# Performance work log

Measured on AMD Instinct MI355X. Metric: run time of the kernel, lower is better.

Reference implementation:

```python
import jax, jax.numpy as jnp
import numpy as np

N_EMBD = 384
HEAD_SIZE = 64
B, T = 16, 2048


def setup_inputs() -> dict:
    key = jax.random.key(0)
    ks = jax.random.split(key, 7)
    s = 1.0 / np.sqrt(N_EMBD)
    return {
        "x": jax.random.normal(ks[0], (B, T, N_EMBD), dtype=jnp.float32),
        "Wq": jax.random.uniform(ks[1], (N_EMBD, HEAD_SIZE), jnp.float32, -s, s),
        "bq": jax.random.uniform(ks[2], (HEAD_SIZE,), jnp.float32, -s, s),
        "Wk": jax.random.uniform(ks[3], (N_EMBD, HEAD_SIZE), jnp.float32, -s, s),
        "bk": jax.random.uniform(ks[4], (HEAD_SIZE,), jnp.float32, -s, s),
        "Wv": jax.random.uniform(ks[5], (N_EMBD, HEAD_SIZE), jnp.float32, -s, s),
        "bv": jax.random.uniform(ks[6], (HEAD_SIZE,), jnp.float32, -s, s),
    }


def reference(x, Wq, bq, Wk, bk, Wv, bv):
    # QKV projections: [B,T,C] @ [C,H] -> [B,T,H]
    q = x @ Wq + bq
    k = x @ Wk + bk
    v = x @ Wv + bv
    scale = k.shape[-1] ** (-0.5)
    # NOTE: original forward applies NO causal mask (tril buffer unused).
    scores = jnp.einsum("bqh,bkh->bqk", q, k) * scale  # [B,T,T]
    wmap = jax.nn.softmax(scores, axis=-1)
    # dropout is identity in eval mode
    out = jnp.einsum("bqk,bkh->bqh", wmap, v)  # [B,T,H]
    return out
```

## Files before the change

### kernel.cpp

```cpp
#include <hip/hip_runtime.h>
#include <hip/hip_bf16.h>
#include <cstdint>

typedef unsigned short u16;
typedef __attribute__((ext_vector_type(8))) short short8;
typedef __attribute__((ext_vector_type(4))) short short4v;
typedef __attribute__((ext_vector_type(4))) float f32x4;

#define MFMA16(a, b, c) __builtin_amdgcn_mfma_f32_16x16x32_bf16((a), (b), (c), 0, 0, 0)

constexpr int Bn   = 16;
constexpr int Tn   = 2048;
constexpr int Cn   = 384;
constexpr int Hn   = 64;
constexpr long NTOK = (long)Bn * Tn;
constexpr long NELT = NTOK * Hn;
constexpr int SPLITS = 4;
constexpr int NT_PER = 32 / SPLITS;

#define QSCALE 0.18033688011112042f

__device__ __forceinline__ u16 f2bf(float f) {
  union { float f; uint32_t u; } c; c.f = f;
  uint32_t u = c.u;
  return (u16)((u + 0x7fffu + ((u >> 16) & 1u)) >> 16);
}

__device__ __forceinline__ uint32_t pkbf(float a, float b) {
  uint32_t d;
  asm("v_cvt_pk_bf16_f32 %0, %1, %2" : "=v"(d) : "v"(a), "v"(b));
  return d;
}

__device__ __forceinline__ short8 ldx8(const float* p) {
  const float4 f0 = *reinterpret_cast<const float4*>(p);
  const float4 f1 = *reinterpret_cast<const float4*>(p + 4);
  union { short8 s8; uint32_t u[4]; } r;
  r.u[0] = pkbf(f0.x, f0.y); r.u[1] = pkbf(f0.z, f0.w);
  r.u[2] = pkbf(f1.x, f1.y); r.u[3] = pkbf(f1.z, f1.w);
  return r.s8;
}

__device__ __forceinline__ void gl16(const u16* g, const u16* l) {
  __builtin_amdgcn_global_load_lds(
      (const __attribute__((address_space(1))) void*)g,
      (__attribute__((address_space(3))) void*)l, 16, 0, 0);
}

__global__ __launch_bounds__(256) void wtrans(
    const float* __restrict__ Wq, const float* __restrict__ Wk,
    const float* __restrict__ Wv, u16* __restrict__ wtd)
{
  __shared__ u16 tile[64][65];
  const int m  = blockIdx.x / 6;
  const int kc = blockIdx.x % 6;
  const float* W = (m == 0) ? Wq : (m == 1) ? Wk : Wv;
  const int t = threadIdx.x;

  {
    const int kr = t >> 2, seg = t & 3;
    const float* src = W + (size_t)(kc * 64 + kr) * Hn + seg * 16;
    #pragma unroll
    for (int j = 0; j < 4; ++j) {
      const float4 f = *reinterpret_cast<const float4*>(src + j * 4);
      u16* p = &tile[kr][seg * 16 + j * 4];
      p[0] = f2bf(f.x); p[1] = f2bf(f.y); p[2] = f2bf(f.z); p[3] = f2bf(f.w);
    }
  }
  __syncthreads();
  {
    const int hr = t >> 2, seg = t & 3;
    union { short8 s; u16 u[8]; } o0, o1;
    #pragma unroll
    for (int j = 0; j < 8; ++j) o0.u[j] = tile[seg * 16 + j][hr];
    #pragma unroll
    for (int j = 0; j < 8; ++j) o1.u[j] = tile[seg * 16 + 8 + j][hr];
    u16* dst = wtd + ((size_t)m * 64 + hr) * Cn + kc * 64 + seg * 16;
    *reinterpret_cast<short8*>(dst)     = o0.s;
    *reinterpret_cast<short8*>(dst + 8) = o1.s;
  }
}

__global__ __launch_bounds__(256, 2) void qkv_proj(
    const float* __restrict__ x, const u16* __restrict__ wtd,
    const float* __restrict__ bq, const float* __restrict__ bk,
    const float* __restrict__ bv,
    u16* __restrict__ oq, u16* __restrict__ ok, u16* __restrict__ ovt)
{
  __shared__ u16 wbuf[3][3 * 64 * 64];

  const int t    = threadIdx.x;
  const int lane = t & 63;
  const int w    = t >> 6;
  const int l15  = lane & 15;
  const int lh   = lane >> 4;
  const long r0  = (long)blockIdx.x * 64;

  int srcoff[6];
  #pragma unroll
  for (int i = 0; i < 6; ++i) {
    const int g = i * 256 + t;
    const int r = g >> 3, c = g & 7;
    srcoff[i] = r * Cn + ((c ^ (r & 7)) << 3);
  }
  const int ldsb = w * 64 * 8;

  const float* xrow = x + (r0 + w * 16 + l15) * Cn;

  short8 aCur0 = ldx8(xrow + lh * 8);
  short8 aCur1 = ldx8(xrow + 32 + lh * 8);
  short8 aNxt0, aNxt1;

  const int cks0 = ((lh)     ^ (l15 & 7)) << 3;
  const int cks1 = ((lh + 4) ^ (l15 & 7)) << 3;

  f32x4 acc[3][4];
  #pragma unroll
  for (int m = 0; m < 3; ++m)
    #pragma unroll
    for (int n = 0; n < 4; ++n) acc[m][n] = f32x4{0.f, 0.f, 0.f, 0.f};

  #pragma unroll
  for (int i = 0; i < 6; ++i)
    gl16(wtd + srcoff[i], &wbuf[0][(i * 256) * 8 + ldsb]);
  #pragma unroll
  for (int i = 0; i < 6; ++i)
    gl16(wtd + 64 + srcoff[i], &wbuf[1][(i * 256) * 8 + ldsb]);
  asm volatile("s_waitcnt vmcnt(6)" ::: "memory");
  __builtin_amdgcn_s_barrier();
  __builtin_amdgcn_sched_barrier(0);

  for (int kc = 0; kc < 6; ++kc) {
    const int cb = kc % 3;
    const int sb = (kc + 2) % 3;
    if (kc + 2 < 6) {
      #pragma unroll
      for (int i = 0; i < 6; ++i)
        gl16(wtd + (kc + 2) * 64 + srcoff[i], &wbuf[sb][(i * 256) * 8 + ldsb]);
    }
    if (kc + 1 < 6) {
      const float* p = xrow + (kc + 1) * 64 + lh * 8;
      aNxt0 = ldx8(p);
      aNxt1 = ldx8(p + 32);
    }

    const u16* wc = &wbuf[cb][0];
    #pragma unroll
    for (int m = 0; m < 3; ++m)
      #pragma unroll
      for (int n = 0; n < 4; ++n) {
        const int row = m * 64 + n * 16 + l15;
        const short8 b0 = *reinterpret_cast<const short8*>(&wc[row * 64 + cks0]);
        acc[m][n] = MFMA16(aCur0, b0, acc[m][n]);
        const short8 b1 = *reinterpret_cast<const short8*>(&wc[row * 64 + cks1]);
        acc[m][n] = MFMA16(aCur1, b1, acc[m][n]);
      }

    if (kc + 1 < 6) {
      if (kc + 2 < 6) asm volatile("s_waitcnt vmcnt(10)" ::: "memory");
      else            asm volatile("s_waitcnt vmcnt(4)"  ::: "memory");
      __builtin_amdgcn_s_barrier();
      __builtin_amdgcn_sched_barrier(0);
      aCur0 = aNxt0;
      aCur1 = aNxt1;
    }
  }

  {
    const float* bias[2] = {bq, bk};
    u16*         dst[2]  = {oq, ok};
    const float  scl[2]  = {QSCALE, 1.0f};
    #pragma unroll
    for (int m = 0; m < 2; ++m) {
      #pragma unroll
      for (int n = 0; n < 4; ++n) {
        int col = n * 16 + l15;
        float bb = bias[m][col];
        #pragma unroll
        for (int r = 0; r < 4; ++r) {
          int row = lh * 4 + r;
          dst[m][(r0 + w * 16 + row) * Hn + col] = f2bf((acc[m][n][r] + bb) * scl[m]);
        }
      }
    }
  }
  {
    const long g    = r0 + w * 16 + lh * 4;
    const long bidx = g >> 11;
    const long tloc = g & 2047;
    const int  u    = (int)(tloc & 63);
    const long tb   = tloc & ~63L;
    const int  slotb = 32 * ((u >> 5) & 1) + 8 * ((u >> 2) & 3) + 4 * ((u >> 4) & 1);
    #pragma unroll
    for (int n = 0; n < 4; ++n) {
      int col = n * 16 + l15;
      float bb = bv[col];
      short4v pk;
      #pragma unroll
      for (int r = 0; r < 4; ++r) pk[r] = (short)f2bf(acc[2][n][r] + bb);
      *reinterpret_cast<short4v*>(ovt + (bidx * Hn + col) * Tn + tb + slotb) = pk;
    }
  }
}

__global__ __launch_bounds__(256, 3) void flash_attn(
    const u16* __restrict__ q, const u16* __restrict__ k,
    const u16* __restrict__ vt, float* __restrict__ opart,
    float* __restrict__ lpart)
{
  __shared__ u16 kbuf[3][64 * 64];
  __shared__ u16 vbuf[3][64 * 64];

  const int t    = threadIdx.x;
  const int lane = t & 63;
  const int w    = t >> 6;
  const int l15  = lane & 15;
  const int lh   = lane >> 4;
  const int swz_id = ((blockIdx.x & 7) << 7) | (blockIdx.x >> 3);
  const int qt    = swz_id & 15;
  const int split = (swz_id >> 4) & (SPLITS - 1);
  const int b     = swz_id >> 6;
  const long rowbase = (long)b * Tn + qt * 128;
  const int it0 = split * NT_PER, it1 = it0 + NT_PER;

  short8 aq[2][2];
  #pragma unroll
  for (int qg = 0; qg < 2; ++qg) {
    const u16* qrow = q + (rowbase + w * 32 + qg * 16 + l15) * Hn;
    aq[qg][0] = *reinterpret_cast<const short8*>(qrow + lh * 8);
    aq[qg][1] = *reinterpret_cast<const short8*>(qrow + 32 + lh * 8);
  }

  f32x4 o[2][4];
  #pragma unroll
  for (int qg = 0; qg < 2; ++qg)
    #pragma unroll
    for (int m = 0; m < 4; ++m) o[qg][m] = f32x4{0.f, 0.f, 0.f, 0.f};
  float lacc[2] = {0.f, 0.f};

  const u16* kb_g = k  + (long)b * Tn * Hn;
  const u16* vb_g = vt + (long)b * Hn * Tn;

  const int g0 = t, g1 = 256 + t;
  const int r0g = g0 >> 3, c0g = g0 & 7;
  const int r1g = g1 >> 3, c1g = g1 & 7;
  const long ksrc0 = (long)r0g * Hn + ((c0g ^ (r0g & 7)) << 3);
  const long ksrc1 = (long)r1g * Hn + ((c1g ^ (r1g & 7)) << 3);
  const long vsrc0 = (long)r0g * Tn + ((c0g ^ (r0g & 7)) << 3);
  const long vsrc1 = (long)r1g * Tn + ((c1g ^ (r1g & 7)) << 3);
  const int wb0 = w * 64 * 8;
  const int wb1 = wb0 + 256 * 8;

  const int swz  = l15 & 7;
  const int cks0 = ((0 * 4 + lh) ^ swz) << 3;
  const int cks1 = ((1 * 4 + lh) ^ swz) << 3;
  const int rfr  = l15 * 64;

  {
    const u16* kt = kb_g + (long)it0 * 64 * Hn;
    const u16* vp = vb_g + it0 * 64;
    gl16(kt + ksrc0, &kbuf[0][wb0]);
    gl16(kt + ksrc1, &kbuf[0][wb1]);
    gl16(vp + vsrc0, &vbuf[0][wb0]);
    gl16(vp + vsrc1, &vbuf[0][wb1]);
    const u16* kt1 = kb_g + (long)(it0 + 1) * 64 * Hn;
    const u16* vp1 = vb_g + (it0 + 1) * 64;
    gl16(kt1 + ksrc0, &kbuf[1][wb0]);
    gl16(kt1 + ksrc1, &kbuf[1][wb1]);
    gl16(vp1 + vsrc0, &vbuf[1][wb0]);
    gl16(vp1 + vsrc1, &vbuf[1][wb1]);
  }
  asm volatile("s_waitcnt vmcnt(4)" ::: "memory");
  __builtin_amdgcn_s_barrier();
  __builtin_amdgcn_sched_barrier(0);

  for (int it = it0; it < it1; ++it) {
    const int cb = (it - it0) % 3;
    const int sb = (it - it0 + 2) % 3;
    if (it + 2 < it1) {
      const u16* kt = kb_g + (long)(it + 2) * 64 * Hn;
      const u16* vp = vb_g + (it + 2) * 64;
      gl16(kt + ksrc0, &kbuf[sb][wb0]);
      gl16(kt + ksrc1, &kbuf[sb][wb1]);
      gl16(vp + vsrc0, &vbuf[sb][wb0]);
      gl16(vp + vsrc1, &vbuf[sb][wb1]);
    }

    const u16* kc  = &kbuf[cb][0];
    const u16* vcb = &vbuf[cb][0];

    f32x4 s0[4], s1[4];
    #pragma unroll
    for (int n = 0; n < 4; ++n) { s0[n] = f32x4{0.f,0.f,0.f,0.f}; s1[n] = f32x4{0.f,0.f,0.f,0.f}; }
    #pragma unroll
    for (int n = 0; n < 4; ++n) {
      const short8 ak0 = *reinterpret_cast<const short8*>(&kc[n * 1024 + rfr + cks0]);
      const short8 ak1 = *reinterpret_cast<const short8*>(&kc[n * 1024 + rfr + cks1]);
      s0[n] = MFMA16(ak0, aq[0][0], s0[n]);
      s0[n] = MFMA16(ak1, aq[0][1], s0[n]);
      s1[n] = MFMA16(ak0, aq[1][0], s1[n]);
      s1[n] = MFMA16(ak1, aq[1][1], s1[n]);
    }

    #pragma unroll
    for (int n = 0; n < 4; ++n)
      #pragma unroll
      for (int r = 0; r < 4; ++r) {
        s0[n][r] = __builtin_amdgcn_exp2f(s0[n][r]);
        s1[n][r] = __builtin_amdgcn_exp2f(s1[n][r]);
      }

    {
      float a0 = (s0[0][0]+s0[0][1])+(s0[0][2]+s0[0][3]);
      float a1 = (s0[1][0]+s0[1][1])+(s0[1][2]+s0[1][3]);
      float a2 = (s0[2][0]+s0[2][1])+(s0[2][2]+s0[2][3]);
      float a3 = (s0[3][0]+s0[3][1])+(s0[3][2]+s0[3][3]);
      lacc[0] += (a0 + a1) + (a2 + a3);
      float b0 = (s1[0][0]+s1[0][1])+(s1[0][2]+s1[0][3]);
      float b1 = (s1[1][0]+s1[1][1])+(s1[1][2]+s1[1][3]);
      float b2 = (s1[2][0]+s1[2][1])+(s1[2][2]+s1[2][3]);
      float b3 = (s1[3][0]+s1[3][1])+(s1[3][2]+s1[3][3]);
      lacc[1] += (b0 + b1) + (b2 + b3);
    }

    union { short8 s8; uint32_t u[4]; } B00, B01, B10, B11;
    B00.u[0] = pkbf(s0[0][0], s0[0][1]); B00.u[1] = pkbf(s0[0][2], s0[0][3]);
    B00.u[2] = pkbf(s0[1][0], s0[1][1]); B00.u[3] = pkbf(s0[1][2], s0[1][3]);
    B01.u[0] = pkbf(s0[2][0], s0[2][1]); B01.u[1] = pkbf(s0[2][2], s0[2][3]);
    B01.u[2] = pkbf(s0[3][0], s0[3][1]); B01.u[3] = pkbf(s0[3][2], s0[3][3]);
    B10.u[0] = pkbf(s1[0][0], s1[0][1]); B10.u[1] = pkbf(s1[0][2], s1[0][3]);
    B10.u[2] = pkbf(s1[1][0], s1[1][1]); B10.u[3] = pkbf(s1[1][2], s1[1][3]);
    B11.u[0] = pkbf(s1[2][0], s1[2][1]); B11.u[1] = pkbf(s1[2][2], s1[2][3]);
    B11.u[2] = pkbf(s1[3][0], s1[3][1]); B11.u[3] = pkbf(s1[3][2], s1[3][3]);

    #pragma unroll
    for (int m = 0; m < 4; ++m) {
      const short8 av0 = *reinterpret_cast<const short8*>(&vcb[m * 1024 + rfr + cks0]);
      const short8 av1 = *reinterpret_cast<const short8*>(&vcb[m * 1024 + rfr + cks1]);
      o[0][m] = MFMA16(av0, B00.s8, o[0][m]);
      o[0][m] = MFMA16(av1, B01.s8, o[0][m]);
      o[1][m] = MFMA16(av0, B10.s8, o[1][m]);
      o[1][m] = MFMA16(av1, B11.s8, o[1][m]);
    }

    if (it + 1 < it1) {
      if (it + 2 < it1) asm volatile("s_waitcnt vmcnt(4)" ::: "memory");
      else              asm volatile("s_waitcnt vmcnt(0)" ::: "memory");
      __builtin_amdgcn_s_barrier();
      __builtin_amdgcn_sched_barrier(0);
    }
  }

  #pragma unroll
  for (int qg = 0; qg < 2; ++qg) {
    float tot = lacc[qg];
    tot += __shfl_xor(tot, 16);
    tot += __shfl_xor(tot, 32);
    const long qrow = rowbase + w * 32 + qg * 16 + l15;
    float* od = opart + ((long)split * NELT) + qrow * Hn;
    #pragma unroll
    for (int m = 0; m < 4; ++m) {
      float4 vv;
      vv.x = o[qg][m][0]; vv.y = o[qg][m][1]; vv.z = o[qg][m][2]; vv.w = o[qg][m][3];
      *reinterpret_cast<float4*>(od + m * 16 + lh * 4) = vv;
    }
    if (lh == 0) lpart[(long)split * NTOK + qrow] = tot;
  }
}

__global__ __launch_bounds__(256) void combine(
    const float* __restrict__ op, const float* __restrict__ lp,
    float* __restrict__ out)
{
  const long idx  = (long)blockIdx.x * 256 + threadIdx.x;
  const long base = idx * 4;
  const long row  = base >> 6;
  float4 acc = *reinterpret_cast<const float4*>(op + base);
  float lsum = lp[row];
  #pragma unroll
  for (int s = 1; s < SPLITS; ++s) {
    const float4 c = *reinterpret_cast<const float4*>(op + s * NELT + base);
    acc.x += c.x; acc.y += c.y; acc.z += c.z; acc.w += c.w;
    lsum += lp[s * NTOK + row];
  }
  const float linv = 1.0f / lsum;
  float4 r;
  r.x = acc.x * linv; r.y = acc.y * linv; r.z = acc.z * linv; r.w = acc.w * linv;
  *reinterpret_cast<float4*>(out + base) = r;
}

extern "C" void kernel_launch(void* const* d_in, const int* in_sizes, int n_in,
                              void* d_out, int out_size, void* d_ws, size_t ws_size,
                              hipStream_t stream) {
  const float* x  = (const float*)d_in[0];
  const float* Wq = (const float*)d_in[1];
  const float* bq = (const float*)d_in[2];
  const float* Wk = (const float*)d_in[3];
  const float* bk = (const float*)d_in[4];
  const float* Wv = (const float*)d_in[5];
  const float* bv = (const float*)d_in[6];
  float* out = (float*)d_out;

  u16* qs  = (u16*)d_ws;
  u16* ks  = qs + NELT;
  u16* vs  = ks + NELT;
  u16* wtd = vs + NELT;
  float* op = (float*)(wtd + 3 * 64 * Cn);
  float* lp = op + (long)SPLITS * NELT;

  hipLaunchKernelGGL(wtrans, dim3(18), dim3(256), 0, stream, Wq, Wk, Wv, wtd);
  hipLaunchKernelGGL(qkv_proj, dim3((int)(NTOK / 64)), dim3(256), 0, stream,
                     x, wtd, bq, bk, bv, qs, ks, vs);
  hipLaunchKernelGGL(flash_attn, dim3(16 * 16 * SPLITS), dim3(256), 0, stream,
                     qs, ks, vs, op, lp);
  hipLaunchKernelGGL(combine, dim3((int)(NELT / 4 / 256)), dim3(256), 0, stream,
                     op, lp, out);
}
```

Baseline: 58.86 us.

## Deepen x prefetch in projection and stage V through registers in attention

```diff
diff --git a/kernel.cpp b/kernel.cpp
--- a/kernel.cpp
+++ b/kernel.cpp
@@ -107,26 +107,27 @@
 
   const float* xrow = x + (r0 + w * 16 + l15) * Cn;
 
+  const int cks0 = ((lh)     ^ (l15 & 7)) << 3;
+  const int cks1 = ((lh + 4) ^ (l15 & 7)) << 3;
+
+  f32x4 acc[3][4];
+  #pragma unroll
+  for (int m = 0; m < 3; ++m)
+    #pragma unroll
+    for (int n = 0; n < 4; ++n) acc[m][n] = f32x4{0.f, 0.f, 0.f, 0.f};
+
+  #pragma unroll
+  for (int i = 0; i < 6; ++i)
+    gl16(wtd + srcoff[i], &wbuf[0][(i * 256) * 8 + ldsb]);
   short8 aCur0 = ldx8(xrow + lh * 8);
   short8 aCur1 = ldx8(xrow + 32 + lh * 8);
-  short8 aNxt0, aNxt1;
-
-  const int cks0 = ((lh)     ^ (l15 & 7)) << 3;
-  const int cks1 = ((lh + 4) ^ (l15 & 7)) << 3;
-
-  f32x4 acc[3][4];
-  #pragma unroll
-  for (int m = 0; m < 3; ++m)
-    #pragma unroll
-    for (int n = 0; n < 4; ++n) acc[m][n] = f32x4{0.f, 0.f, 0.f, 0.f};
-
-  #pragma unroll
-  for (int i = 0; i < 6; ++i)
-    gl16(wtd + srcoff[i], &wbuf[0][(i * 256) * 8 + ldsb]);
   #pragma unroll
   for (int i = 0; i < 6; ++i)
     gl16(wtd + 64 + srcoff[i], &wbuf[1][(i * 256) * 8 + ldsb]);
-  asm volatile("s_waitcnt vmcnt(6)" ::: "memory");
+  short8 aNx10 = ldx8(xrow + 64 + lh * 8);
+  short8 aNx11 = ldx8(xrow + 96 + lh * 8);
+  short8 aNx20, aNx21;
+  asm volatile("s_waitcnt vmcnt(14)" ::: "memory");
   __builtin_amdgcn_s_barrier();
   __builtin_amdgcn_sched_barrier(0);
 
@@ -137,11 +138,9 @@
       #pragma unroll
       for (int i = 0; i < 6; ++i)
         gl16(wtd + (kc + 2) * 64 + srcoff[i], &wbuf[sb][(i * 256) * 8 + ldsb]);
-    }
-    if (kc + 1 < 6) {
-      const float* p = xrow + (kc + 1) * 64 + lh * 8;
-      aNxt0 = ldx8(p);
-      aNxt1 = ldx8(p + 32);
+      const float* p = xrow + (kc + 2) * 64 + lh * 8;
+      aNx20 = ldx8(p);
+      aNx21 = ldx8(p + 32);
     }
 
     const u16* wc = &wbuf[cb][0];
@@ -157,12 +156,12 @@
       }
 
     if (kc + 1 < 6) {
-      if (kc + 2 < 6) asm volatile("s_waitcnt vmcnt(10)" ::: "memory");
+      if (kc + 2 < 6) asm volatile("s_waitcnt vmcnt(14)" ::: "memory");
       else            asm volatile("s_waitcnt vmcnt(4)"  ::: "memory");
       __builtin_amdgcn_s_barrier();
       __builtin_amdgcn_sched_barrier(0);
-      aCur0 = aNxt0;
-      aCur1 = aNxt1;
+      aCur0 = aNx10; aCur1 = aNx11;
+      aNx10 = aNx20; aNx11 = aNx21;
     }
   }
 
@@ -203,13 +202,13 @@
   }
 }
 
-__global__ __launch_bounds__(256, 3) void flash_attn(
+__global__ __launch_bounds__(256, 4) void flash_attn(
     const u16* __restrict__ q, const u16* __restrict__ k,
     const u16* __restrict__ vt, float* __restrict__ opart,
     float* __restrict__ lpart)
 {
   __shared__ u16 kbuf[3][64 * 64];
-  __shared__ u16 vbuf[3][64 * 64];
+  __shared__ u16 vbuf[2][64 * 64];
 
   const int t    = threadIdx.x;
   const int lane = t & 63;
@@ -250,6 +249,8 @@
   const long vsrc1 = (long)r1g * Tn + ((c1g ^ (r1g & 7)) << 3);
   const int wb0 = w * 64 * 8;
   const int wb1 = wb0 + 256 * 8;
+  const int vdst0 = (r0g * 8 + c0g) * 8;
+  const int vdst1 = (r1g * 8 + c1g) * 8;
 
   const int swz  = l15 & 7;
   const int cks0 = ((0 * 4 + lh) ^ swz) << 3;
@@ -257,37 +258,40 @@
   const int rfr  = l15 * 64;
 
   {
-    const u16* kt = kb_g + (long)it0 * 64 * Hn;
     const u16* vp = vb_g + it0 * 64;
-    gl16(kt + ksrc0, &kbuf[0][wb0]);
-    gl16(kt + ksrc1, &kbuf[0][wb1]);
-    gl16(vp + vsrc0, &vbuf[0][wb0]);
-    gl16(vp + vsrc1, &vbuf[0][wb1]);
+    const short8 pv0 = *reinterpret_cast<const short8*>(vp + vsrc0);
+    const short8 pv1 = *reinterpret_cast<const short8*>(vp + vsrc1);
+    const u16* kt0 = kb_g + (long)it0 * 64 * Hn;
+    gl16(kt0 + ksrc0, &kbuf[0][wb0]);
+    gl16(kt0 + ksrc1, &kbuf[0][wb1]);
     const u16* kt1 = kb_g + (long)(it0 + 1) * 64 * Hn;
-    const u16* vp1 = vb_g + (it0 + 1) * 64;
     gl16(kt1 + ksrc0, &kbuf[1][wb0]);
     gl16(kt1 + ksrc1, &kbuf[1][wb1]);
-    gl16(vp1 + vsrc0, &vbuf[1][wb0]);
-    gl16(vp1 + vsrc1, &vbuf[1][wb1]);
-  }
-  asm volatile("s_waitcnt vmcnt(4)" ::: "memory");
+    *reinterpret_cast<short8*>(&vbuf[0][vdst0]) = pv0;
+    *reinterpret_cast<short8*>(&vbuf[0][vdst1]) = pv1;
+  }
+  asm volatile("s_waitcnt vmcnt(2) lgkmcnt(0)" ::: "memory");
   __builtin_amdgcn_s_barrier();
   __builtin_amdgcn_sched_barrier(0);
 
   for (int it = it0; it < it1; ++it) {
     const int cb = (it - it0) % 3;
-    const int sb = (it - it0 + 2) % 3;
+    const int vb = (it - it0) & 1;
+    short8 nv0, nv1;
+    const bool pfv = (it + 1 < it1);
+    if (pfv) {
+      const u16* vp = vb_g + (it + 1) * 64;
+      nv0 = *reinterpret_cast<const short8*>(vp + vsrc0);
+      nv1 = *reinterpret_cast<const short8*>(vp + vsrc1);
+    }
     if (it + 2 < it1) {
       const u16* kt = kb_g + (long)(it + 2) * 64 * Hn;
-      const u16* vp = vb_g + (it + 2) * 64;
-      gl16(kt + ksrc0, &kbuf[sb][wb0]);
-      gl16(kt + ksrc1, &kbuf[sb][wb1]);
-      gl16(vp + vsrc0, &vbuf[sb][wb0]);
-      gl16(vp + vsrc1, &vbuf[sb][wb1]);
+      gl16(kt + ksrc0, &kbuf[(it - it0 + 2) % 3][wb0]);
+      gl16(kt + ksrc1, &kbuf[(it - it0 + 2) % 3][wb1]);
     }
 
     const u16* kc  = &kbuf[cb][0];
-    const u16* vcb = &vbuf[cb][0];
+    const u16* vcb = &vbuf[vb][0];
 
     f32x4 s0[4], s1[4];
     #pragma unroll
@@ -343,9 +347,10 @@
       o[1][m] = MFMA16(av1, B11.s8, o[1][m]);
     }
 
-    if (it + 1 < it1) {
-      if (it + 2 < it1) asm volatile("s_waitcnt vmcnt(4)" ::: "memory");
-      else              asm volatile("s_waitcnt vmcnt(0)" ::: "memory");
+    if (pfv) {
+      *reinterpret_cast<short8*>(&vbuf[vb ^ 1][vdst0]) = nv0;
+      *reinterpret_cast<short8*>(&vbuf[vb ^ 1][vdst1]) = nv1;
+      asm volatile("s_waitcnt lgkmcnt(0)" ::: "memory");
       __builtin_amdgcn_s_barrier();
       __builtin_amdgcn_sched_barrier(0);
     }
```

New measurement: 69.58 us. +18.2%, slower.
